# Kernel optimization log

Hardware: AMD Instinct MI355X
Metric: run time of the kernel (lower is better)

The kernel has to match this reference:

```python
import jax, jax.numpy as jnp
import numpy as np

N_NODES = 100000


def _glorot(key, shape):
    fan_in, fan_out = shape[1], shape[0]
    lim = np.sqrt(6.0 / (fan_in + fan_out))
    return jax.random.uniform(key, shape, jnp.float32, -lim, lim)


def setup_inputs() -> dict:
    key = jax.random.key(0)
    ks = jax.random.split(key, 12)
    x = jax.random.normal(ks[0], (N_NODES, 64), jnp.float32)
    edge_index = jax.random.randint(ks[1], (2, 1600000), 0, N_NODES, jnp.int64)
    return {
        "x": x,
        "edge_index": edge_index,
        # SAGEConv layer 1: lin_l (neighbors, with bias), lin_r (root, no bias)
        "W1l": _glorot(ks[2], (64, 64)), "b1": jnp.zeros((64,), jnp.float32), "W1r": _glorot(ks[3], (64, 64)),
        "W2l": _glorot(ks[4], (64, 64)), "b2": jnp.zeros((64,), jnp.float32), "W2r": _glorot(ks[5], (64, 64)),
        "W3l": _glorot(ks[6], (32, 64)), "b3": jnp.zeros((32,), jnp.float32), "W3r": _glorot(ks[7], (32, 64)),
        "Wreg": _glorot(ks[8], (1, 32)), "breg": jnp.zeros((1,), jnp.float32),
    }


def _sage_conv(x, src, dst, Wl, b, Wr):
    # mean aggregation of source-node features at destination nodes
    msg_sum = jax.ops.segment_sum(x[src], dst, num_segments=N_NODES)  # [N, d]
    deg = jax.ops.segment_sum(jnp.ones_like(src, dtype=x.dtype), dst, num_segments=N_NODES)
    mean = msg_sum / jnp.maximum(deg, 1.0)[:, None]
    return mean @ Wl.T + b + x @ Wr.T


def reference(x, edge_index, W1l, b1, W1r, W2l, b2, W2r, W3l, b3, W3r, Wreg, breg):
    src, dst = edge_index[0], edge_index[1]
    h = jax.nn.relu(_sage_conv(x, src, dst, W1l, b1, W1r))
    h = jax.nn.relu(_sage_conv(h, src, dst, W2l, b2, W2r))
    h = jax.nn.relu(_sage_conv(h, src, dst, W3l, b3, W3r))
    return (h @ Wreg.T + breg).squeeze(-1)  # [N]
```

## Files before the change

kernel.cpp:

```cpp
#include <hip/hip_runtime.h>
#include <math.h>

#define N_NODES 100000
#define N_EDGES 1600000
#define NB 782
#define NTILES 6250
#define NPART 256

typedef unsigned int uint;
typedef __attribute__((ext_vector_type(8))) short bf16x8;
typedef __attribute__((ext_vector_type(4))) float f32x4;

__device__ inline ushort f2bf(float f) {
    uint u = __float_as_uint(f);
    uint r = (u + 0x7fffu + ((u >> 16) & 1u)) >> 16;
    return (ushort)r;
}
__device__ inline uint pack2bf(float lo, float hi) {
    return (uint)f2bf(lo) | ((uint)f2bf(hi) << 16);
}

__global__ void misc_kernel(const float* __restrict__ W1l, const float* __restrict__ W1r,
                            const float* __restrict__ W2l, const float* __restrict__ W2r,
                            const float* __restrict__ W3l, const float* __restrict__ W3r,
                            ushort* __restrict__ wf,
                            const float* __restrict__ x, ushort* __restrict__ xb) {
    if (blockIdx.x < 80) {
        int idx = blockIdx.x * 256 + threadIdx.x;
        if (idx >= 20480) return;
        const float *Wl, *Wr;
        int base, KT;
        if (idx < 8192)       { base = 0;     Wl = W1l; Wr = W1r; KT = 128; }
        else if (idx < 16384) { base = 8192;  Wl = W2l; Wr = W2r; KT = 128; }
        else if (idx < 18432) { base = 16384; Wl = W3l; Wr = 0;   KT = 64; }
        else                  { base = 18432; Wl = W3r; Wr = 0;   KT = 64; }
        int r = idx - base;
        int f = r >> 9;
        int l = (r >> 3) & 63;
        int i = r & 7;
        int nks = KT >> 5;
        int nt = f / nks, ks = f - nt * nks;
        int k = ks * 32 + ((l >> 4) << 3) + i;
        int j = nt * 16 + (l & 15);
        float v = (k < 64) ? Wl[j * 64 + k] : Wr[j * 64 + (k - 64)];
        wf[idx] = f2bf(v);
    } else {
        const int n4 = N_NODES * 64 / 4;
        int i0 = (blockIdx.x - 80) * 256 + threadIdx.x;
        for (int i = i0; i < n4; i += 400 * 256) {
            float4 v = ((const float4*)x)[i];
            uint2 o;
            o.x = pack2bf(v.x, v.y);
            o.y = pack2bf(v.z, v.w);
            ((uint2*)xb)[i] = o;
        }
    }
}

__global__ void bucket_hist(const int* __restrict__ dst, int* __restrict__ hist2D, int nE) {
    __shared__ int hist[NB];
    const int PER = (N_EDGES + NPART - 1) / NPART;
    int e0 = blockIdx.x * PER;
    int e1 = min(e0 + PER, nE);
    for (int i = threadIdx.x; i < NB; i += 1024) hist[i] = 0;
    __syncthreads();
    for (int e = e0 + threadIdx.x; e < e1; e += 1024)
        atomicAdd(&hist[dst[e] >> 7], 1);
    __syncthreads();
    for (int i = threadIdx.x; i < NB; i += 1024)
        hist2D[blockIdx.x * NB + i] = hist[i];
}

__global__ void col_scan(const int* __restrict__ hist2D, int* __restrict__ colExcl,
                         int* __restrict__ bucketTot) {
    __shared__ int s[NPART];
    int i = blockIdx.x;
    int v = hist2D[threadIdx.x * NB + i];
    s[threadIdx.x] = v;
    __syncthreads();
    for (int off = 1; off < NPART; off <<= 1) {
        int t = (threadIdx.x >= (unsigned)off) ? s[threadIdx.x - off] : 0;
        __syncthreads();
        s[threadIdx.x] += t;
        __syncthreads();
    }
    colExcl[threadIdx.x * NB + i] = s[threadIdx.x] - v;
    if (threadIdx.x == NPART - 1) bucketTot[i] = s[NPART - 1];
}

__global__ void scan_tot(const int* __restrict__ bucketTot, int* __restrict__ bucketBase) {
    __shared__ int s[1024];
    int tid = threadIdx.x;
    int v = (tid < NB) ? bucketTot[tid] : 0;
    s[tid] = v;
    __syncthreads();
    for (int off = 1; off < 1024; off <<= 1) {
        int t = (tid >= off) ? s[tid - off] : 0;
        __syncthreads();
        s[tid] += t;
        __syncthreads();
    }
    if (tid < NB) bucketBase[tid] = s[tid] - v;
    if (tid == 0) bucketBase[NB] = s[NB - 1];
}

__global__ void partition_kernel(const int* __restrict__ src, const int* __restrict__ dst,
                                 const int* __restrict__ bucketBase, const int* __restrict__ colExcl,
                                 int* __restrict__ part, int nE) {
    __shared__ int base[NB];
    __shared__ int rank[NB];
    const int PER = (N_EDGES + NPART - 1) / NPART;
    int e0 = blockIdx.x * PER;
    int e1 = min(e0 + PER, nE);
    for (int i = threadIdx.x; i < NB; i += 1024) {
        base[i] = bucketBase[i] + colExcl[blockIdx.x * NB + i];
        rank[i] = 0;
    }
    __syncthreads();
    for (int e = e0 + threadIdx.x; e < e1; e += 1024) {
        int d = dst[e];
        int bk = d >> 7;
        int r = atomicAdd(&rank[bk], 1);
        part[base[bk] + r] = src[e] | ((d & 127) << 20);
    }
}

__global__ void bucket_fill2(const int* __restrict__ bucketBase, const int* __restrict__ part,
                             int* __restrict__ col, int* __restrict__ rowptr,
                             float* __restrict__ invdeg, int n) {
    __shared__ int cnt[128];
    __shared__ int cnt2[128];
    __shared__ int exclS[128];
    __shared__ int s[128];
    int b = blockIdx.x;
    int d0 = b << 7;
    int dl = min(128, n - d0);
    int ebeg = bucketBase[b], eend = bucketBase[b + 1];
    if (threadIdx.x < 128) { cnt[threadIdx.x] = 0; cnt2[threadIdx.x] = 0; }
    __syncthreads();
    for (int i = ebeg + (int)threadIdx.x; i < eend; i += 512)
        atomicAdd(&cnt[part[i] >> 20], 1);
    __syncthreads();
    if (threadIdx.x < 128) s[threadIdx.x] = cnt[threadIdx.x];
    __syncthreads();
    for (int off = 1; off < 128; off <<= 1) {
        int t = 0;
        if (threadIdx.x < 128 && threadIdx.x >= (unsigned)off) t = s[threadIdx.x - off];
        __syncthreads();
        if (threadIdx.x < 128) s[threadIdx.x] += t;
        __syncthreads();
    }
    if ((int)threadIdx.x < dl) {
        int c = cnt[threadIdx.x];
        int ex = ebeg + s[threadIdx.x] - c;
        rowptr[d0 + threadIdx.x] = ex;
        invdeg[d0 + threadIdx.x] = 1.0f / fmaxf((float)c, 1.0f);
        exclS[threadIdx.x] = ex;
    }
    if (threadIdx.x == 0 && d0 + dl == n) rowptr[n] = eend;
    __syncthreads();
    for (int i = ebeg + (int)threadIdx.x; i < eend; i += 512) {
        int v = part[i];
        int doff = v >> 20;
        int pos = exclS[doff] + atomicAdd(&cnt2[doff], 1);
        col[pos] = v & 0xFFFFF;
    }
}

__global__ void gather_mean(const ushort* __restrict__ xb, const int* __restrict__ rowptr,
                            const int* __restrict__ col, const float* __restrict__ invdeg,
                            ushort* __restrict__ meanb, int n) {
    int tid = blockIdx.x * blockDim.x + threadIdx.x;
    int wid = tid >> 6;
    int lane = threadIdx.x & 63;
    int grp = lane >> 3;
    int li = lane & 7;
    int node = wid * 8 + grp;
    if (node >= n) return;
    int beg = rowptr[node];
    int end = rowptr[node + 1];
    int fb = li * 8;
    float a0 = 0.f, a1 = 0.f, a2 = 0.f, a3 = 0.f, a4 = 0.f, a5 = 0.f, a6 = 0.f, a7 = 0.f;
    for (int i = beg; i < end; i += 8) {
        int idx = i + li;
        int ci = (idx < end) ? col[idx] : 0;
        int cnt = end - i;
#pragma unroll
        for (int t = 0; t < 8; ++t) {
            if (t < cnt) {
                int s = __shfl(ci, grp * 8 + t, 64);
                uint4 w = *(const uint4*)(xb + (size_t)s * 64 + fb);
                a0 += __uint_as_float(w.x << 16);
                a1 += __uint_as_float(w.x & 0xffff0000u);
                a2 += __uint_as_float(w.y << 16);
                a3 += __uint_as_float(w.y & 0xffff0000u);
                a4 += __uint_as_float(w.z << 16);
                a5 += __uint_as_float(w.z & 0xffff0000u);
                a6 += __uint_as_float(w.w << 16);
                a7 += __uint_as_float(w.w & 0xffff0000u);
            }
        }
    }
    float id = invdeg[node];
    uint4 o;
    o.x = pack2bf(a0 * id, a1 * id);
    o.y = pack2bf(a2 * id, a3 * id);
    o.z = pack2bf(a4 * id, a5 * id);
    o.w = pack2bf(a6 * id, a7 * id);
    *(uint4*)(meanb + (size_t)node * 64 + fb) = o;
}

__global__ void gather_mean32(const ushort* __restrict__ gb, const int* __restrict__ rowptr,
                              const int* __restrict__ col, const float* __restrict__ invdeg,
                              ushort* __restrict__ mean32b, int n) {
    int tid = blockIdx.x * blockDim.x + threadIdx.x;
    int wid = tid >> 6;
    int lane = threadIdx.x & 63;
    int grp = lane >> 2;
    int li = lane & 3;
    int node = wid * 16 + grp;
    if (node >= n) return;
    int beg = rowptr[node];
    int end = rowptr[node + 1];
    int fb = li * 8;
    float a0 = 0.f, a1 = 0.f, a2 = 0.f, a3 = 0.f, a4 = 0.f, a5 = 0.f, a6 = 0.f, a7 = 0.f;
    for (int i = beg; i < end; i += 4) {
        int idx = i + li;
        int ci = (idx < end) ? col[idx] : 0;
        int cnt = end - i;
#pragma unroll
        for (int t = 0; t < 4; ++t) {
            if (t < cnt) {
                int s = __shfl(ci, grp * 4 + t, 64);
                uint4 w = *(const uint4*)(gb + (size_t)s * 32 + fb);
                a0 += __uint_as_float(w.x << 16);
                a1 += __uint_as_float(w.x & 0xffff0000u);
                a2 += __uint_as_float(w.y << 16);
                a3 += __uint_as_float(w.y & 0xffff0000u);
                a4 += __uint_as_float(w.z << 16);
                a5 += __uint_as_float(w.z & 0xffff0000u);
                a6 += __uint_as_float(w.w << 16);
                a7 += __uint_as_float(w.w & 0xffff0000u);
            }
        }
    }
    float id = invdeg[node];
    uint4 o;
    o.x = pack2bf(a0 * id, a1 * id);
    o.y = pack2bf(a2 * id, a3 * id);
    o.z = pack2bf(a4 * id, a5 * id);
    o.w = pack2bf(a6 * id, a7 * id);
    *(uint4*)(mean32b + (size_t)node * 32 + fb) = o;
}

__global__ void __launch_bounds__(256)
mfma_transform(const ushort* __restrict__ rootb, const ushort* __restrict__ meanb,
               const ushort* __restrict__ wfrag, const float* __restrict__ bias,
               ushort* __restrict__ outb, int ntiles) {
    int wave = threadIdx.x >> 6;
    int lane = threadIdx.x & 63;

    bf16x8 wf[4][4];
#pragma unroll
    for (int nt = 0; nt < 4; ++nt)
#pragma unroll
        for (int ks = 0; ks < 4; ++ks)
            wf[nt][ks] = *(const bf16x8*)(wfrag + (size_t)((nt * 4 + ks) * 64 + lane) * 8);

    float bl[4];
#pragma unroll
    for (int nt = 0; nt < 4; ++nt) bl[nt] = bias[nt * 16 + (lane & 15)];

    int arow = lane & 15;
    int koff = (lane >> 4) * 8;
    int crow = (lane >> 4) * 4;
    int nwaves = gridDim.x * 4;

    for (int tile = blockIdx.x * 4 + wave; tile < ntiles; tile += nwaves) {
        int n0 = tile * 16;
        const ushort* mrow = meanb + (size_t)(n0 + arow) * 64 + koff;
        const ushort* xrow = rootb + (size_t)(n0 + arow) * 64 + koff;
        bf16x8 a0 = *(const bf16x8*)(mrow);
        bf16x8 a1 = *(const bf16x8*)(mrow + 32);
        bf16x8 a2 = *(const bf16x8*)(xrow);
        bf16x8 a3 = *(const bf16x8*)(xrow + 32);
#pragma unroll
        for (int nt = 0; nt < 4; ++nt) {
            f32x4 c = {0.f, 0.f, 0.f, 0.f};
            c = __builtin_amdgcn_mfma_f32_16x16x32_bf16(a0, wf[nt][0], c, 0, 0, 0);
            c = __builtin_amdgcn_mfma_f32_16x16x32_bf16(a1, wf[nt][1], c, 0, 0, 0);
            c = __builtin_amdgcn_mfma_f32_16x16x32_bf16(a2, wf[nt][2], c, 0, 0, 0);
            c = __builtin_amdgcn_mfma_f32_16x16x32_bf16(a3, wf[nt][3], c, 0, 0, 0);
#pragma unroll
            for (int i = 0; i < 4; ++i) {
                float v = fmaxf(c[i] + bl[nt], 0.0f);
                outb[(size_t)(n0 + crow + i) * 64 + nt * 16 + (lane & 15)] = f2bf(v);
            }
        }
    }
}

__global__ void __launch_bounds__(256)
mfma_pretrans3(const ushort* __restrict__ hb, const ushort* __restrict__ wfrag,
               ushort* __restrict__ gb, int ntiles) {
    int wave = threadIdx.x >> 6;
    int lane = threadIdx.x & 63;

    bf16x8 wf[2][2];
#pragma unroll
    for (int nt = 0; nt < 2; ++nt)
#pragma unroll
        for (int ks = 0; ks < 2; ++ks)
            wf[nt][ks] = *(const bf16x8*)(wfrag + (size_t)((nt * 2 + ks) * 64 + lane) * 8);

    int arow = lane & 15;
    int koff = (lane >> 4) * 8;
    int crow = (lane >> 4) * 4;
    int nwaves = gridDim.x * 4;

    for (int tile = blockIdx.x * 4 + wave; tile < ntiles; tile += nwaves) {
        int n0 = tile * 16;
        const ushort* hrow = hb + (size_t)(n0 + arow) * 64 + koff;
        bf16x8 a0 = *(const bf16x8*)(hrow);
        bf16x8 a1 = *(const bf16x8*)(hrow + 32);
#pragma unroll
        for (int nt = 0; nt < 2; ++nt) {
            f32x4 c = {0.f, 0.f, 0.f, 0.f};
            c = __builtin_amdgcn_mfma_f32_16x16x32_bf16(a0, wf[nt][0], c, 0, 0, 0);
            c = __builtin_amdgcn_mfma_f32_16x16x32_bf16(a1, wf[nt][1], c, 0, 0, 0);
#pragma unroll
            for (int i = 0; i < 4; ++i)
                gb[(size_t)(n0 + crow + i) * 32 + nt * 16 + (lane & 15)] = f2bf(c[i]);
        }
    }
}

__global__ void __launch_bounds__(256)
mfma_t3(const ushort* __restrict__ hb, const ushort* __restrict__ mean32b,
        const ushort* __restrict__ wfrag, const float* __restrict__ b3,
        const float* __restrict__ Wreg, const float* __restrict__ breg,
        float* __restrict__ out, int ntiles) {
    int wave = threadIdx.x >> 6;
    int lane = threadIdx.x & 63;

    bf16x8 wf[2][2];
#pragma unroll
    for (int nt = 0; nt < 2; ++nt)
#pragma unroll
        for (int ks = 0; ks < 2; ++ks)
            wf[nt][ks] = *(const bf16x8*)(wfrag + (size_t)((nt * 2 + ks) * 64 + lane) * 8);

    float bl[2], wr[2];
#pragma unroll
    for (int nt = 0; nt < 2; ++nt) {
        bl[nt] = b3[nt * 16 + (lane & 15)];
        wr[nt] = Wreg[nt * 16 + (lane & 15)];
    }
    float br = breg[0];

    int arow = lane & 15;
    int koff = (lane >> 4) * 8;
    int crow = (lane >> 4) * 4;
    int nwaves = gridDim.x * 4;

    for (int tile = blockIdx.x * 4 + wave; tile < ntiles; tile += nwaves) {
        int n0 = tile * 16;
        const ushort* hrow = hb + (size_t)(n0 + arow) * 64 + koff;
        bf16x8 a0 = *(const bf16x8*)(hrow);
        bf16x8 a1 = *(const bf16x8*)(hrow + 32);
        float part0 = 0.f, part1 = 0.f, part2 = 0.f, part3 = 0.f;
#pragma unroll
        for (int nt = 0; nt < 2; ++nt) {
            f32x4 c = {0.f, 0.f, 0.f, 0.f};
            c = __builtin_amdgcn_mfma_f32_16x16x32_bf16(a0, wf[nt][0], c, 0, 0, 0);
            c = __builtin_amdgcn_mfma_f32_16x16x32_bf16(a1, wf[nt][1], c, 0, 0, 0);
#pragma unroll
            for (int i = 0; i < 4; ++i) {
                ushort mw = mean32b[(size_t)(n0 + crow + i) * 32 + nt * 16 + (lane & 15)];
                float m = __uint_as_float((uint)mw << 16);
                float v = fmaxf(c[i] + bl[nt] + m, 0.0f) * wr[nt];
                if (i == 0) part0 += v;
                else if (i == 1) part1 += v;
                else if (i == 2) part2 += v;
                else part3 += v;
            }
        }
#pragma unroll
        for (int s = 1; s < 16; s <<= 1) {
            part0 += __shfl_xor(part0, s, 64);
            part1 += __shfl_xor(part1, s, 64);
            part2 += __shfl_xor(part2, s, 64);
            part3 += __shfl_xor(part3, s, 64);
        }
        if ((lane & 15) == 0) {
            float4 o;
            o.x = part0 + br; o.y = part1 + br; o.z = part2 + br; o.w = part3 + br;
            *(float4*)(out + n0 + crow) = o;
        }
    }
}

extern "C" void kernel_launch(void* const* d_in, const int* in_sizes, int n_in,
                              void* d_out, int out_size, void* d_ws, size_t ws_size,
                              hipStream_t stream) {
    const float* x    = (const float*)d_in[0];
    const int*   ei   = (const int*)d_in[1];
    const float* W1l  = (const float*)d_in[2];
    const float* b1   = (const float*)d_in[3];
    const float* W1r  = (const float*)d_in[4];
    const float* W2l  = (const float*)d_in[5];
    const float* b2   = (const float*)d_in[6];
    const float* W2r  = (const float*)d_in[7];
    const float* W3l  = (const float*)d_in[8];
    const float* b3   = (const float*)d_in[9];
    const float* W3r  = (const float*)d_in[10];
    const float* Wreg = (const float*)d_in[11];
    const float* breg = (const float*)d_in[12];

    const int* src = ei;
    const int* dst = ei + N_EDGES;

    char* p = (char*)d_ws;
    auto alloc = [&](size_t bytes) {
        char* r = p;
        p += (bytes + 255) & ~(size_t)255;
        return r;
    };
    int*    hist2D    = (int*)alloc((size_t)NPART * NB * sizeof(int));
    int*    colExcl   = (int*)alloc((size_t)NPART * NB * sizeof(int));
    int*    bucketTot = (int*)alloc(NB * sizeof(int));
    int*    bucketBase= (int*)alloc((NB + 1) * sizeof(int));
    int*    rowptr    = (int*)alloc((N_NODES + 1) * sizeof(int));
    int*    col       = (int*)alloc((size_t)N_EDGES * sizeof(int));
    float*  invdeg    = (float*)alloc(N_NODES * sizeof(float));
    ushort* wfrag     = (ushort*)alloc(20480 * sizeof(ushort));
    char*   slot   = (char*)alloc((size_t)N_EDGES * sizeof(int));
    int*    part   = (int*)slot;
    ushort* gb     = (ushort*)slot;
    ushort* xb     = (ushort*)alloc((size_t)N_NODES * 64 * sizeof(ushort));
    ushort* meanb  = (ushort*)alloc((size_t)N_NODES * 64 * sizeof(ushort));
    ushort* mean32b= meanb;
    ushort* hb     = (ushort*)alloc((size_t)N_NODES * 64 * sizeof(ushort));
    float*  out    = (float*)d_out;

    const int TB = 256;
    int g64Blocks    = (N_NODES * 8 + TB - 1) / TB;
    int g32Blocks    = (N_NODES * 4 + TB - 1) / TB;
    const int mfmaBlocks = 512;

    misc_kernel<<<480, 256, 0, stream>>>(W1l, W1r, W2l, W2r, W3l, W3r, wfrag, x, xb);
    bucket_hist<<<NPART, 1024, 0, stream>>>(dst, hist2D, N_EDGES);
    col_scan<<<NB, NPART, 0, stream>>>(hist2D, colExcl, bucketTot);
    scan_tot<<<1, 1024, 0, stream>>>(bucketTot, bucketBase);
    partition_kernel<<<NPART, 1024, 0, stream>>>(src, dst, bucketBase, colExcl, part, N_EDGES);
    bucket_fill2<<<NB, 512, 0, stream>>>(bucketBase, part, col, rowptr, invdeg, N_NODES);

    gather_mean<<<g64Blocks, 256, 0, stream>>>(xb, rowptr, col, invdeg, meanb, N_NODES);
    mfma_transform<<<mfmaBlocks, 256, 0, stream>>>(xb, meanb, wfrag + 0, b1, hb, NTILES);

    gather_mean<<<g64Blocks, 256, 0, stream>>>(hb, rowptr, col, invdeg, meanb, N_NODES);
    mfma_transform<<<mfmaBlocks, 256, 0, stream>>>(hb, meanb, wfrag + 8192, b2, hb, NTILES);

    mfma_pretrans3<<<mfmaBlocks, 256, 0, stream>>>(hb, wfrag + 16384, gb, NTILES);
    gather_mean32<<<g32Blocks, 256, 0, stream>>>(gb, rowptr, col, invdeg, mean32b, N_NODES);
    mfma_t3<<<mfmaBlocks, 256, 0, stream>>>(hb, mean32b, wfrag + 18432, b3, Wreg, breg, out, NTILES);
}
```

Before: 169.0 us.

## Fuse neighbor mean gather into MFMA layer kernels and merge histogram into prep kernel

Each SAGE layer's mean-aggregation gather now runs inside the MFMA transform kernel. It writes the per-block mean tile to shared memory rather than to a global buffer that a second kernel then reads back. The bucket histogram is folded into the weight/feature conversion kernel as extra blocks, which removes launches. Layer 2 writes to a separate h2b buffer because its gather reads hb from arbitrary nodes, so it can no longer work in place. The cost is less latency hiding: each block's gather and MFMA phases are now serialized behind a barrier.

```diff
diff --git a/kernel.cpp b/kernel.cpp
--- a/kernel.cpp
+++ b/kernel.cpp
@@ -20,11 +20,12 @@
     return (uint)f2bf(lo) | ((uint)f2bf(hi) << 16);
 }
 
-__global__ void misc_kernel(const float* __restrict__ W1l, const float* __restrict__ W1r,
-                            const float* __restrict__ W2l, const float* __restrict__ W2r,
-                            const float* __restrict__ W3l, const float* __restrict__ W3r,
-                            ushort* __restrict__ wf,
-                            const float* __restrict__ x, ushort* __restrict__ xb) {
+__global__ void misc_hist(const float* __restrict__ W1l, const float* __restrict__ W1r,
+                          const float* __restrict__ W2l, const float* __restrict__ W2r,
+                          const float* __restrict__ W3l, const float* __restrict__ W3r,
+                          ushort* __restrict__ wf,
+                          const float* __restrict__ x, ushort* __restrict__ xb,
+                          const int* __restrict__ dst, int* __restrict__ hist2D) {
     if (blockIdx.x < 80) {
         int idx = blockIdx.x * 256 + threadIdx.x;
         if (idx >= 20480) return;
@@ -44,7 +45,7 @@
         int j = nt * 16 + (l & 15);
         float v = (k < 64) ? Wl[j * 64 + k] : Wr[j * 64 + (k - 64)];
         wf[idx] = f2bf(v);
-    } else {
+    } else if (blockIdx.x < 480) {
         const int n4 = N_NODES * 64 / 4;
         int i0 = (blockIdx.x - 80) * 256 + threadIdx.x;
         for (int i = i0; i < n4; i += 400 * 256) {
@@ -54,21 +55,20 @@
             o.y = pack2bf(v.z, v.w);
             ((uint2*)xb)[i] = o;
         }
-    }
-}
-
-__global__ void bucket_hist(const int* __restrict__ dst, int* __restrict__ hist2D, int nE) {
-    __shared__ int hist[NB];
-    const int PER = (N_EDGES + NPART - 1) / NPART;
-    int e0 = blockIdx.x * PER;
-    int e1 = min(e0 + PER, nE);
-    for (int i = threadIdx.x; i < NB; i += 1024) hist[i] = 0;
-    __syncthreads();
-    for (int e = e0 + threadIdx.x; e < e1; e += 1024)
-        atomicAdd(&hist[dst[e] >> 7], 1);
-    __syncthreads();
-    for (int i = threadIdx.x; i < NB; i += 1024)
-        hist2D[blockIdx.x * NB + i] = hist[i];
+    } else {
+        __shared__ int hist[NB];
+        int hb_i = blockIdx.x - 480;
+        const int PER = (N_EDGES + NPART - 1) / NPART;
+        int e0 = hb_i * PER;
+        int e1 = min(e0 + PER, N_EDGES);
+        for (int i = threadIdx.x; i < NB; i += 256) hist[i] = 0;
+        __syncthreads();
+        for (int e = e0 + (int)threadIdx.x; e < e1; e += 256)
+            atomicAdd(&hist[dst[e] >> 7], 1);
+        __syncthreads();
+        for (int i = threadIdx.x; i < NB; i += 256)
+            hist2D[hb_i * NB + i] = hist[i];
+    }
 }
 
 __global__ void col_scan(const int* __restrict__ hist2D, int* __restrict__ colExcl,
@@ -117,7 +117,7 @@
         rank[i] = 0;
     }
     __syncthreads();
-    for (int e = e0 + threadIdx.x; e < e1; e += 1024) {
+    for (int e = e0 + (int)threadIdx.x; e < e1; e += 1024) {
         int d = dst[e];
         int bk = d >> 7;
         int r = atomicAdd(&rank[bk], 1);
@@ -167,97 +167,13 @@
     }
 }
 
-__global__ void gather_mean(const ushort* __restrict__ xb, const int* __restrict__ rowptr,
-                            const int* __restrict__ col, const float* __restrict__ invdeg,
-                            ushort* __restrict__ meanb, int n) {
-    int tid = blockIdx.x * blockDim.x + threadIdx.x;
-    int wid = tid >> 6;
-    int lane = threadIdx.x & 63;
-    int grp = lane >> 3;
-    int li = lane & 7;
-    int node = wid * 8 + grp;
-    if (node >= n) return;
-    int beg = rowptr[node];
-    int end = rowptr[node + 1];
-    int fb = li * 8;
-    float a0 = 0.f, a1 = 0.f, a2 = 0.f, a3 = 0.f, a4 = 0.f, a5 = 0.f, a6 = 0.f, a7 = 0.f;
-    for (int i = beg; i < end; i += 8) {
-        int idx = i + li;
-        int ci = (idx < end) ? col[idx] : 0;
-        int cnt = end - i;
-#pragma unroll
-        for (int t = 0; t < 8; ++t) {
-            if (t < cnt) {
-                int s = __shfl(ci, grp * 8 + t, 64);
-                uint4 w = *(const uint4*)(xb + (size_t)s * 64 + fb);
-                a0 += __uint_as_float(w.x << 16);
-                a1 += __uint_as_float(w.x & 0xffff0000u);
-                a2 += __uint_as_float(w.y << 16);
-                a3 += __uint_as_float(w.y & 0xffff0000u);
-                a4 += __uint_as_float(w.z << 16);
-                a5 += __uint_as_float(w.z & 0xffff0000u);
-                a6 += __uint_as_float(w.w << 16);
-                a7 += __uint_as_float(w.w & 0xffff0000u);
-            }
-        }
-    }
-    float id = invdeg[node];
-    uint4 o;
-    o.x = pack2bf(a0 * id, a1 * id);
-    o.y = pack2bf(a2 * id, a3 * id);
-    o.z = pack2bf(a4 * id, a5 * id);
-    o.w = pack2bf(a6 * id, a7 * id);
-    *(uint4*)(meanb + (size_t)node * 64 + fb) = o;
-}
-
-__global__ void gather_mean32(const ushort* __restrict__ gb, const int* __restrict__ rowptr,
-                              const int* __restrict__ col, const float* __restrict__ invdeg,
-                              ushort* __restrict__ mean32b, int n) {
-    int tid = blockIdx.x * blockDim.x + threadIdx.x;
-    int wid = tid >> 6;
-    int lane = threadIdx.x & 63;
-    int grp = lane >> 2;
-    int li = lane & 3;
-    int node = wid * 16 + grp;
-    if (node >= n) return;
-    int beg = rowptr[node];
-    int end = rowptr[node + 1];
-    int fb = li * 8;
-    float a0 = 0.f, a1 = 0.f, a2 = 0.f, a3 = 0.f, a4 = 0.f, a5 = 0.f, a6 = 0.f, a7 = 0.f;
-    for (int i = beg; i < end; i += 4) {
-        int idx = i + li;
-        int ci = (idx < end) ? col[idx] : 0;
-        int cnt = end - i;
-#pragma unroll
-        for (int t = 0; t < 4; ++t) {
-            if (t < cnt) {
-                int s = __shfl(ci, grp * 4 + t, 64);
-                uint4 w = *(const uint4*)(gb + (size_t)s * 32 + fb);
-                a0 += __uint_as_float(w.x << 16);
-                a1 += __uint_as_float(w.x & 0xffff0000u);
-                a2 += __uint_as_float(w.y << 16);
-                a3 += __uint_as_float(w.y & 0xffff0000u);
-                a4 += __uint_as_float(w.z << 16);
-                a5 += __uint_as_float(w.z & 0xffff0000u);
-                a6 += __uint_as_float(w.w << 16);
-                a7 += __uint_as_float(w.w & 0xffff0000u);
-            }
-        }
-    }
-    float id = invdeg[node];
-    uint4 o;
-    o.x = pack2bf(a0 * id, a1 * id);
-    o.y = pack2bf(a2 * id, a3 * id);
-    o.z = pack2bf(a4 * id, a5 * id);
-    o.w = pack2bf(a6 * id, a7 * id);
-    *(uint4*)(mean32b + (size_t)node * 32 + fb) = o;
-}
-
 __global__ void __launch_bounds__(256)
-mfma_transform(const ushort* __restrict__ rootb, const ushort* __restrict__ meanb,
-               const ushort* __restrict__ wfrag, const float* __restrict__ bias,
-               ushort* __restrict__ outb, int ntiles) {
-    int wave = threadIdx.x >> 6;
+fused_layer(const ushort* __restrict__ rootb, const int* __restrict__ rowptr,
+            const int* __restrict__ col, const float* __restrict__ invdeg,
+            const ushort* __restrict__ wfrag, const float* __restrict__ bias,
+            ushort* __restrict__ outb, int n) {
+    __shared__ __align__(16) ushort smean[64 * 64];
+    int w = threadIdx.x >> 6;
     int lane = threadIdx.x & 63;
 
     bf16x8 wf[4][4];
@@ -266,36 +182,75 @@
 #pragma unroll
         for (int ks = 0; ks < 4; ++ks)
             wf[nt][ks] = *(const bf16x8*)(wfrag + (size_t)((nt * 4 + ks) * 64 + lane) * 8);
-
     float bl[4];
 #pragma unroll
     for (int nt = 0; nt < 4; ++nt) bl[nt] = bias[nt * 16 + (lane & 15)];
 
+    int grp8 = lane >> 3;
+    int li8 = lane & 7;
+    int fb = li8 * 8;
+
+#pragma unroll
+    for (int p = 0; p < 2; ++p) {
+        int row = w * 16 + p * 8 + grp8;
+        int node = blockIdx.x * 64 + row;
+        if (node < n) {
+            int beg = rowptr[node];
+            int end = rowptr[node + 1];
+            float a0 = 0.f, a1 = 0.f, a2 = 0.f, a3 = 0.f, a4 = 0.f, a5 = 0.f, a6 = 0.f, a7 = 0.f;
+            for (int i = beg; i < end; i += 8) {
+                int idx = i + li8;
+                int ci = (idx < end) ? col[idx] : 0;
+                int cnt = end - i;
+#pragma unroll
+                for (int t = 0; t < 8; ++t) {
+                    if (t < cnt) {
+                        int s = __shfl(ci, grp8 * 8 + t, 64);
+                        uint4 wv = *(const uint4*)(rootb + (size_t)s * 64 + fb);
+                        a0 += __uint_as_float(wv.x << 16);
+                        a1 += __uint_as_float(wv.x & 0xffff0000u);
+                        a2 += __uint_as_float(wv.y << 16);
+                        a3 += __uint_as_float(wv.y & 0xffff0000u);
+                        a4 += __uint_as_float(wv.z << 16);
+                        a5 += __uint_as_float(wv.z & 0xffff0000u);
+                        a6 += __uint_as_float(wv.w << 16);
+                        a7 += __uint_as_float(wv.w & 0xffff0000u);
+                    }
+                }
+            }
+            float id = invdeg[node];
+            uint4 o;
+            o.x = pack2bf(a0 * id, a1 * id);
+            o.y = pack2bf(a2 * id, a3 * id);
+            o.z = pack2bf(a4 * id, a5 * id);
+            o.w = pack2bf(a6 * id, a7 * id);
+            *(uint4*)(smean + row * 64 + fb) = o;
+        }
+    }
+    __syncthreads();
+
+    int n0 = blockIdx.x * 64 + w * 16;
+    if (n0 >= n) return;
     int arow = lane & 15;
     int koff = (lane >> 4) * 8;
     int crow = (lane >> 4) * 4;
-    int nwaves = gridDim.x * 4;
-
-    for (int tile = blockIdx.x * 4 + wave; tile < ntiles; tile += nwaves) {
-        int n0 = tile * 16;
-        const ushort* mrow = meanb + (size_t)(n0 + arow) * 64 + koff;
-        const ushort* xrow = rootb + (size_t)(n0 + arow) * 64 + koff;
-        bf16x8 a0 = *(const bf16x8*)(mrow);
-        bf16x8 a1 = *(const bf16x8*)(mrow + 32);
-        bf16x8 a2 = *(const bf16x8*)(xrow);
-        bf16x8 a3 = *(const bf16x8*)(xrow + 32);
-#pragma unroll
-        for (int nt = 0; nt < 4; ++nt) {
-            f32x4 c = {0.f, 0.f, 0.f, 0.f};
-            c = __builtin_amdgcn_mfma_f32_16x16x32_bf16(a0, wf[nt][0], c, 0, 0, 0);
-            c = __builtin_amdgcn_mfma_f32_16x16x32_bf16(a1, wf[nt][1], c, 0, 0, 0);
-            c = __builtin_amdgcn_mfma_f32_16x16x32_bf16(a2, wf[nt][2], c, 0, 0, 0);
-            c = __builtin_amdgcn_mfma_f32_16x16x32_bf16(a3, wf[nt][3], c, 0, 0, 0);
-#pragma unroll
-            for (int i = 0; i < 4; ++i) {
-                float v = fmaxf(c[i] + bl[nt], 0.0f);
-                outb[(size_t)(n0 + crow + i) * 64 + nt * 16 + (lane & 15)] = f2bf(v);
-            }
+
+    bf16x8 a0 = *(const bf16x8*)(smean + (w * 16 + arow) * 64 + koff);
+    bf16x8 a1 = *(const bf16x8*)(smean + (w * 16 + arow) * 64 + koff + 32);
+    const ushort* xrow = rootb + (size_t)(n0 + arow) * 64 + koff;
+    bf16x8 a2 = *(const bf16x8*)(xrow);
+    bf16x8 a3 = *(const bf16x8*)(xrow + 32);
+#pragma unroll
+    for (int nt = 0; nt < 4; ++nt) {
+        f32x4 c = {0.f, 0.f, 0.f, 0.f};
+        c = __builtin_amdgcn_mfma_f32_16x16x32_bf16(a0, wf[nt][0], c, 0, 0, 0);
+        c = __builtin_amdgcn_mfma_f32_16x16x32_bf16(a1, wf[nt][1], c, 0, 0, 0);
+        c = __builtin_amdgcn_mfma_f32_16x16x32_bf16(a2, wf[nt][2], c, 0, 0, 0);
+        c = __builtin_amdgcn_mfma_f32_16x16x32_bf16(a3, wf[nt][3], c, 0, 0, 0);
+#pragma unroll
+        for (int i = 0; i < 4; ++i) {
+            float v = fmaxf(c[i] + bl[nt], 0.0f);
+            outb[(size_t)(n0 + crow + i) * 64 + nt * 16 + (lane & 15)] = f2bf(v);
         }
     }
 }
@@ -336,11 +291,14 @@
 }
 
 __global__ void __launch_bounds__(256)
-mfma_t3(const ushort* __restrict__ hb, const ushort* __restrict__ mean32b,
-        const ushort* __restrict__ wfrag, const float* __restrict__ b3,
-        const float* __restrict__ Wreg, const float* __restrict__ breg,
-        float* __restrict__ out, int ntiles) {
-    int wave = threadIdx.x >> 6;
+fused_l3(const ushort* __restrict__ hb, const ushort* __restrict__ gb,
+         const int* __restrict__ rowptr, const int* __restrict__ col,
+         const float* __restrict__ invdeg,
+         const ushort* __restrict__ wfrag, const float* __restrict__ b3,
+         const float* __restrict__ Wreg, const float* __restrict__ breg,
+         float* __restrict__ out, int n) {
+    __shared__ __align__(16) ushort smean[64 * 32];
+    int w = threadIdx.x >> 6;
     int lane = threadIdx.x & 63;
 
     bf16x8 wf[2][2];
@@ -349,7 +307,6 @@
 #pragma unroll
         for (int ks = 0; ks < 2; ++ks)
             wf[nt][ks] = *(const bf16x8*)(wfrag + (size_t)((nt * 2 + ks) * 64 + lane) * 8);
-
     float bl[2], wr[2];
 #pragma unroll
     for (int nt = 0; nt < 2; ++nt) {
@@ -358,45 +315,82 @@
     }
     float br = breg[0];
 
+    int grp4 = lane >> 2;
+    int li4 = lane & 3;
+    int fb = li4 * 8;
+    int row = w * 16 + grp4;
+    int node = blockIdx.x * 64 + row;
+    if (node < n) {
+        int beg = rowptr[node];
+        int end = rowptr[node + 1];
+        float a0 = 0.f, a1 = 0.f, a2 = 0.f, a3 = 0.f, a4 = 0.f, a5 = 0.f, a6 = 0.f, a7 = 0.f;
+        for (int i = beg; i < end; i += 4) {
+            int idx = i + li4;
+            int ci = (idx < end) ? col[idx] : 0;
+            int cnt = end - i;
+#pragma unroll
+            for (int t = 0; t < 4; ++t) {
+                if (t < cnt) {
+                    int s = __shfl(ci, grp4 * 4 + t, 64);
+                    uint4 wv = *(const uint4*)(gb + (size_t)s * 32 + fb);
+                    a0 += __uint_as_float(wv.x << 16);
+                    a1 += __uint_as_float(wv.x & 0xffff0000u);
+                    a2 += __uint_as_float(wv.y << 16);
+                    a3 += __uint_as_float(wv.y & 0xffff0000u);
+                    a4 += __uint_as_float(wv.z << 16);
+                    a5 += __uint_as_float(wv.z & 0xffff0000u);
+                    a6 += __uint_as_float(wv.w << 16);
+                    a7 += __uint_as_float(wv.w & 0xffff0000u);
+                }
+            }
+        }
+        float id = invdeg[node];
+        uint4 o;
+        o.x = pack2bf(a0 * id, a1 * id);
+        o.y = pack2bf(a2 * id, a3 * id);
+        o.z = pack2bf(a4 * id, a5 * id);
+        o.w = pack2bf(a6 * id, a7 * id);
+        *(uint4*)(smean + row * 32 + fb) = o;
+    }
+    __syncthreads();
+
+    int n0 = blockIdx.x * 64 + w * 16;
+    if (n0 >= n) return;
     int arow = lane & 15;
     int koff = (lane >> 4) * 8;
     int crow = (lane >> 4) * 4;
-    int nwaves = gridDim.x * 4;
-
-    for (int tile = blockIdx.x * 4 + wave; tile < ntiles; tile += nwaves) {
-        int n0 = tile * 16;
-        const ushort* hrow = hb + (size_t)(n0 + arow) * 64 + koff;
-        bf16x8 a0 = *(const bf16x8*)(hrow);
-        bf16x8 a1 = *(const bf16x8*)(hrow + 32);
-        float part0 = 0.f, part1 = 0.f, part2 = 0.f, part3 = 0.f;
-#pragma unroll
-        for (int nt = 0; nt < 2; ++nt) {
-            f32x4 c = {0.f, 0.f, 0.f, 0.f};
-            c = __builtin_amdgcn_mfma_f32_16x16x32_bf16(a0, wf[nt][0], c, 0, 0, 0);
-            c = __builtin_amdgcn_mfma_f32_16x16x32_bf16(a1, wf[nt][1], c, 0, 0, 0);
-#pragma unroll
-            for (int i = 0; i < 4; ++i) {
-                ushort mw = mean32b[(size_t)(n0 + crow + i) * 32 + nt * 16 + (lane & 15)];
-                float m = __uint_as_float((uint)mw << 16);
-                float v = fmaxf(c[i] + bl[nt] + m, 0.0f) * wr[nt];
-                if (i == 0) part0 += v;
-                else if (i == 1) part1 += v;
-                else if (i == 2) part2 += v;
-                else part3 += v;
-            }
-        }
-#pragma unroll
-        for (int s = 1; s < 16; s <<= 1) {
-            part0 += __shfl_xor(part0, s, 64);
-            part1 += __shfl_xor(part1, s, 64);
-            part2 += __shfl_xor(part2, s, 64);
-            part3 += __shfl_xor(part3, s, 64);
-        }
-        if ((lane & 15) == 0) {
-            float4 o;
-            o.x = part0 + br; o.y = part1 + br; o.z = part2 + br; o.w = part3 + br;
-            *(float4*)(out + n0 + crow) = o;
-        }
+
+    const ushort* hrow = hb + (size_t)(n0 + arow) * 64 + koff;
+    bf16x8 a0 = *(const bf16x8*)(hrow);
+    bf16x8 a1 = *(const bf16x8*)(hrow + 32);
+    float part0 = 0.f, part1 = 0.f, part2 = 0.f, part3 = 0.f;
+#pragma unroll
+    for (int nt = 0; nt < 2; ++nt) {
+        f32x4 c = {0.f, 0.f, 0.f, 0.f};
+        c = __builtin_amdgcn_mfma_f32_16x16x32_bf16(a0, wf[nt][0], c, 0, 0, 0);
+        c = __builtin_amdgcn_mfma_f32_16x16x32_bf16(a1, wf[nt][1], c, 0, 0, 0);
+#pragma unroll
+        for (int i = 0; i < 4; ++i) {
+            ushort mw = smean[(w * 16 + crow + i) * 32 + nt * 16 + (lane & 15)];
+            float m = __uint_as_float((uint)mw << 16);
+            float v = fmaxf(c[i] + bl[nt] + m, 0.0f) * wr[nt];
+            if (i == 0) part0 += v;
+            else if (i == 1) part1 += v;
+            else if (i == 2) part2 += v;
+            else part3 += v;
+        }
+    }
+#pragma unroll
+    for (int s = 1; s < 16; s <<= 1) {
+        part0 += __shfl_xor(part0, s, 64);
+        part1 += __shfl_xor(part1, s, 64);
+        part2 += __shfl_xor(part2, s, 64);
+        part3 += __shfl_xor(part3, s, 64);
+    }
+    if ((lane & 15) == 0) {
+        float4 o;
+        o.x = part0 + br; o.y = part1 + br; o.z = part2 + br; o.w = part3 + br;
+        *(float4*)(out + n0 + crow) = o;
     }
 }
 
@@ -438,30 +432,23 @@
     int*    part   = (int*)slot;
     ushort* gb     = (ushort*)slot;
     ushort* xb     = (ushort*)alloc((size_t)N_NODES * 64 * sizeof(ushort));
-    ushort* meanb  = (ushort*)alloc((size_t)N_NODES * 64 * sizeof(ushort));
-    ushort* mean32b= meanb;
     ushort* hb     = (ushort*)alloc((size_t)N_NODES * 64 * sizeof(ushort));
+    ushort* h2b    = (ushort*)alloc((size_t)N_NODES * 64 * sizeof(ushort));
     float*  out    = (float*)d_out;
 
-    const int TB = 256;
-    int g64Blocks    = (N_NODES * 8 + TB - 1) / TB;
-    int g32Blocks    = (N_NODES * 4 + TB - 1) / TB;
-    const int mfmaBlocks = 512;
-
-    misc_kernel<<<480, 256, 0, stream>>>(W1l, W1r, W2l, W2r, W3l, W3r, wfrag, x, xb);
-    bucket_hist<<<NPART, 1024, 0, stream>>>(dst, hist2D, N_EDGES);
+    int fusedBlocks = (N_NODES + 63) / 64;
+
+    misc_hist<<<736, 256, 0, stream>>>(W1l, W1r, W2l, W2r, W3l, W3r, wfrag, x, xb, dst, hist2D);
     col_scan<<<NB, NPART, 0, stream>>>(hist2D, colExcl, bucketTot);
     scan_tot<<<1, 1024, 0, stream>>>(bucketTot, bucketBase);
     partition_kernel<<<NPART, 1024, 0, stream>>>(src, dst, bucketBase, colExcl, part, N_EDGES);
     bucket_fill2<<<NB, 512, 0, stream>>>(bucketBase, part, col, rowptr, invdeg, N_NODES);
 
-    gather_mean<<<g64Blocks, 256, 0, stream>>>(xb, rowptr, col, invdeg, meanb, N_NODES);
-    mfma_transform<<<mfmaBlocks, 256, 0, stream>>>(xb, meanb, wfrag + 0, b1, hb, NTILES);
-
-    gather_mean<<<g64Blocks, 256, 0, stream>>>(hb, rowptr, col, invdeg, meanb, N_NODES);
-    mfma_transform<<<mfmaBlocks, 256, 0, stream>>>(hb, meanb, wfrag + 8192, b2, hb, NTILES);
-
-    mfma_pretrans3<<<mfmaBlocks, 256, 0, stream>>>(hb, wfrag + 16384, gb, NTILES);
-    gather_mean32<<<g32Blocks, 256, 0, stream>>>(gb, rowptr, col, invdeg, mean32b, N_NODES);
-    mfma_t3<<<mfmaBlocks, 256, 0, stream>>>(hb, mean32b, wfrag + 18432, b3, Wreg, breg, out, NTILES);
-}
+    fused_layer<<<fusedBlocks, 256, 0, stream>>>(xb, rowptr, col, invdeg, wfrag + 0, b1, hb, N_NODES);
+
+    fused_layer<<<fusedBlocks, 256, 0, stream>>>(hb, rowptr, col, invdeg, wfrag + 8192, b2, h2b, N_NODES);
+
+    mfma_pretrans3<<<512, 256, 0, stream>>>(h2b, wfrag + 16384, gb, NTILES);
+    fused_l3<<<fusedBlocks, 256, 0, stream>>>(h2b, gb, rowptr, col, invdeg,
+                                              wfrag + 18432, b3, Wreg, breg, out, N_NODES);
+}
```

New measurement: 189.8 us. +12.3%, slower.
